# Performance work log

Hardware: AMD Instinct MI355X
Metric: run time of the kernel (lower is better)

Reference implementation:

```python
import jax, jax.numpy as jnp
import numpy as np

RTOL, ATOL = 1e-3, 1e-6
MAX_STEPS = 20          # fixed upper bound on adaptive steps (masked scan)
TA, TB, TC = 1.0, 1.0, 0.0  # trig basis params a, b, c from basis_str
B, DIN, DT, DOUT = 512, 512, 512, 512


def _rms(x):
    return jnp.sqrt(jnp.mean(x * x))


def _ode_f(t, A, C):
    # Basis.trig: stack([sin(a*A + b*t + c), cos(a*A + b*t + c)], -1) -> [B, DT, 2]
    phase = TA * A + TB * t + TC
    basis = jnp.stack([jnp.sin(phase), jnp.cos(phase)], axis=-1)
    # tensordot(A_basis, C, dims=([1,2], [1,2])): contract tensor dims + basis dim
    return jnp.einsum('bjk,ijk->bi', basis, C)


def _rk45(C, y0, t0, t1):
    """scipy-style adaptive RK45 (Dormand-Prince) from t0 to t1, fixed-length masked scan."""
    f = lambda t, y: _ode_f(t, y, C)
    f0 = f(t0, y0)
    # --- scipy _select_initial_step ---
    scale0 = ATOL + RTOL * jnp.abs(y0)
    d0 = _rms(y0 / scale0)
    d1 = _rms(f0 / scale0)
    h0 = jnp.where((d0 < 1e-5) | (d1 < 1e-5), jnp.float32(1e-6), 0.01 * d0 / d1)
    f1 = f(t0 + h0, y0 + h0 * f0)
    d2 = _rms((f1 - f0) / scale0) / h0
    dmax = jnp.maximum(d1, d2)
    h1 = jnp.where(dmax <= 1e-15, jnp.maximum(jnp.float32(1e-6), h0 * 1e-3), (0.01 / dmax) ** 0.2)
    h_init = jnp.minimum(jnp.minimum(100.0 * h0, h1), t1 - t0)

    def step(carry, _):
        t, y, fy, h, done = carry
        hs = jnp.minimum(h, t1 - t)
        k1 = fy
        k2 = f(t + hs * (1.0 / 5.0), y + hs * (k1 * (1.0 / 5.0)))
        k3 = f(t + hs * (3.0 / 10.0), y + hs * (3.0 / 40.0 * k1 + 9.0 / 40.0 * k2))
        k4 = f(t + hs * (4.0 / 5.0), y + hs * (44.0 / 45.0 * k1 - 56.0 / 15.0 * k2 + 32.0 / 9.0 * k3))
        k5 = f(t + hs * (8.0 / 9.0), y + hs * (19372.0 / 6561.0 * k1 - 25360.0 / 2187.0 * k2
                                               + 64448.0 / 6561.0 * k3 - 212.0 / 729.0 * k4))
        k6 = f(t + hs, y + hs * (9017.0 / 3168.0 * k1 - 355.0 / 33.0 * k2 + 46732.0 / 5247.0 * k3
                                 + 49.0 / 176.0 * k4 - 5103.0 / 18656.0 * k5))
        y_new = y + hs * (35.0 / 384.0 * k1 + 500.0 / 1113.0 * k3 + 125.0 / 192.0 * k4
                          - 2187.0 / 6784.0 * k5 + 11.0 / 84.0 * k6)
        k7 = f(t + hs, y_new)  # FSAL stage
        err = hs * (71.0 / 57600.0 * k1 - 71.0 / 16695.0 * k3 + 71.0 / 1920.0 * k4
                    - 17253.0 / 339200.0 * k5 + 22.0 / 525.0 * k6 - 1.0 / 40.0 * k7)
        sc = ATOL + RTOL * jnp.maximum(jnp.abs(y), jnp.abs(y_new))
        en = _rms(err / sc)
        accept = en < 1.0
        safe = jnp.maximum(en, 1e-10)
        fac = jnp.where(accept,
                        jnp.minimum(10.0, 0.9 * safe ** -0.2),
                        jnp.maximum(0.2, 0.9 * safe ** -0.2))
        t_n = jnp.where(accept, t + hs, t)
        y_n = jnp.where(accept, y_new, y)
        f_n = jnp.where(accept, k7, fy)
        h_n = hs * fac
        reached = t_n >= t1 - 1e-7
        # freeze state once integration is finished
        t_o = jnp.where(done, t, t_n)
        y_o = jnp.where(done, y, y_n)
        f_o = jnp.where(done, fy, f_n)
        h_o = jnp.where(done, h, h_n)
        return (t_o, y_o, f_o, h_o, done | reached), None

    init = (jnp.float32(t0), y0, f0, h_init.astype(jnp.float32), jnp.array(False))
    (tf, yf, _, _, _), _ = jax.lax.scan(step, init, None, length=MAX_STEPS)
    return yf


def setup_inputs() -> dict:
    key = jax.random.key(0)
    kx, kp, kc, kf = jax.random.split(key, 4)
    x = jax.random.normal(kx, (B, DIN), dtype=jnp.float32)
    P = jax.random.uniform(kp, (DIN, DT), dtype=jnp.float32, minval=0.01, maxval=1.0)
    # scale C so dA/dt stays O(1) at DT=512 (pure rescaling of the Uniform init)
    C = jax.random.uniform(kc, (DT, DT, 2), dtype=jnp.float32, minval=0.01, maxval=1.0) / (DT * 2)
    F = jax.random.uniform(kf, (DT, DOUT), dtype=jnp.float32, minval=0.01, maxval=1.0)
    return {"x": x, "P": P, "C": C, "F": F}


def reference(x, P, C, F):
    # A0 = tensordot(x, P) over input dims
    A0 = jnp.einsum('bi,ij->bj', x, P)
    Af = _rk45(C, A0, jnp.float32(0.0), jnp.float32(1.0))
    # y_hat = tensordot(A_f, F) over tensor dims
    return jnp.einsum('bj,jo->bo', Af, F)
```

## Files before the change

kernel.cpp:

```cpp
#include <hip/hip_runtime.h>
#include <cmath>

typedef float floatx4 __attribute__((ext_vector_type(4)));
typedef __bf16 bf16x8 __attribute__((ext_vector_type(8)));
typedef unsigned uintx4 __attribute__((ext_vector_type(4)));

#define NDT 512
#define NELF 262144.0f

#define AF0_OFF 16384
#define AF1_OFF (16384 + 262144)
#define BFC_OFF (16384 + 2 * 262144)
#define BFP_OFF (BFC_OFF + 262144)
#define BFF_OFF (BFP_OFF + 131072)

#define RTOLc 1e-3f
#define ATOLc 1e-6f
#define TAc 1.0f
#define TBc 1.0f
#define TCc 0.0f

union UB { uint4 u; bf16x8 v; };
union UB2 { unsigned long long q[2]; uint4 u; bf16x8 v; uintx4 x; };

__device__ __forceinline__ uint32_t f2bf(float f) {
  uint32_t u = __float_as_uint(f);
  return (u + 0x7fffu + ((u >> 16) & 1u)) >> 16;
}

#define AST(p, v) __hip_atomic_store((p), (v), __ATOMIC_RELAXED, __HIP_MEMORY_SCOPE_AGENT)
#define ALD(p) __hip_atomic_load((p), __ATOMIC_RELAXED, __HIP_MEMORY_SCOPE_AGENT)

__device__ __forceinline__ uintx4 ld128_x(const void* p) {
  uintx4 r;
  asm volatile("global_load_dwordx4 %0, %1, off sc0\n\ts_waitcnt vmcnt(0)"
               : "=v"(r) : "v"(p) : "memory");
  return r;
}

__global__ __launch_bounds__(256) void pack_all(const float* __restrict__ C,
                                                const float* __restrict__ P,
                                                const float* __restrict__ F,
                                                __bf16* __restrict__ BfC,
                                                unsigned* __restrict__ BfP,
                                                unsigned* __restrict__ BfF,
                                                unsigned* __restrict__ ctl) {
  const int bid = blockIdx.x, tid = threadIdx.x;
  if (bid == 0) {
    for (int i = tid; i < 10240; i += 256) ctl[i] = 0u;
  }
  if (bid < 512) {
    int t = bid * 256 + tid;
    int i = t >> 8;
    int pr = t & 255;
    floatx4 v = *(const floatx4*)(C + (size_t)i * 1024 + pr * 4);
    uint32_t w0 = f2bf(v[0]) | (f2bf(v[1]) << 16);
    uint32_t w1 = f2bf(v[2]) | (f2bf(v[3]) << 16);
    int c0 = i >> 4;
    int kc = pr >> 3;
    int lq = (pr >> 1) & 3;
    int ln = (i & 15) | (lq << 4);
    int jp = (pr & 1) * 4;
    uint2 val; val.x = w0; val.y = w1;
    *(uint2*)(BfC + ((size_t)(c0 * 32 + kc) * 64 + ln) * 8 + jp) = val;
  } else {
    const float* M = (bid < 640) ? P : F;
    unsigned* Bf = (bid < 640) ? BfP : BfF;
    int t = ((bid < 640) ? (bid - 512) : (bid - 640)) * 256 + tid;
    int lane = t & 63;
    int kc = (t >> 6) & 15;
    int nf = t >> 10;
    int n = nf * 16 + (lane & 15);
    int K0 = kc * 32 + ((lane >> 4) & 3) * 8;
    const float* mp = M + (size_t)K0 * NDT + n;
    uint32_t e0 = f2bf(mp[0]);
    uint32_t e1 = f2bf(mp[512]);
    uint32_t e2 = f2bf(mp[1024]);
    uint32_t e3 = f2bf(mp[1536]);
    uint32_t e4 = f2bf(mp[2048]);
    uint32_t e5 = f2bf(mp[2560]);
    uint32_t e6 = f2bf(mp[3072]);
    uint32_t e7 = f2bf(mp[3584]);
    *(uint4*)(Bf + ((size_t)(nf * 16 + kc) * 64 + lane) * 4) =
        make_uint4(e0 | (e1 << 16), e2 | (e3 << 16), e4 | (e5 << 16), e6 | (e7 << 16));
  }
}

__global__ __launch_bounds__(256, 1) void ode_mfma(const float* __restrict__ x,
                                                   float* __restrict__ out,
                                                   float* __restrict__ ws) {
  __shared__ __align__(16) float red[2][4][16][68];
  __shared__ __align__(16) unsigned short ldsX[16 * 64 * 8];
  __shared__ float bred[4];
  __shared__ float shb0s, shb1s;
  __shared__ unsigned sxc[8];

  unsigned* FLAG = (unsigned*)ws;
  float* PART1 = ws + 4096;
  unsigned long long* AfA = (unsigned long long*)(ws + AF0_OFF);
  unsigned long long* AfB = (unsigned long long*)(ws + AF1_OFF);
  unsigned long long* YF = (unsigned long long*)(ws + AF0_OFF);
  const __bf16* Bf = (const __bf16*)(ws + BFC_OFF);
  const __bf16* BfP = (const __bf16*)(ws + BFP_OFF);
  const __bf16* BfF = (const __bf16*)(ws + BFF_OFF);

  const int tid = threadIdx.x;
  const int lane = tid & 63;
  const int w = tid >> 6;
  const int cb = blockIdx.x >> 5;
  const int rg = blockIdx.x & 31;
  const int rl = tid & 15;
  const int gcq = cb * 16 + (tid >> 4);
  const int blk = rg * 8 + cb;

  bool fastp;
  {
    unsigned myxcc;
    asm volatile("s_getreg_b32 %0, hwreg(HW_REG_XCC_ID)" : "=s"(myxcc));
    myxcc &= 15u;
    if (tid == 0) AST(&FLAG[blk * 8 + 4], myxcc + 1u);
    if (tid < 8) {
      unsigned v;
      while ((v = ALD(&FLAG[(rg * 8 + tid) * 8 + 4])) == 0u) __builtin_amdgcn_s_sleep(1);
      sxc[tid] = v;
    }
    __syncthreads();
    fastp = true;
#pragma unroll
    for (int i = 0; i < 8; ++i) fastp = fastp && (sxc[i] == sxc[0]);
  }

  UB Breg[4][8];
#pragma unroll
  for (int cf = 0; cf < 4; ++cf)
#pragma unroll
    for (int i = 0; i < 8; ++i)
      Breg[cf][i].u =
          *(const uint4*)(Bf + (((size_t)(cb * 4 + cf) * 32 + 8 * w + i) * 64 + lane) * 8);

  int rg_phase = 0, par = 0, r4p = 0;

  auto rg_barrier = [&]() {
    __syncthreads();
    ++rg_phase;
    if (tid == 0) AST(&FLAG[blk * 8], (unsigned)rg_phase);
    if (tid < 8) {
      while (ALD(&FLAG[(rg * 8 + tid) * 8]) < (unsigned)rg_phase) __builtin_amdgcn_s_sleep(1);
    }
    __syncthreads();
  };

  auto reduce4 = [&](floatx4 a0, floatx4 a1, floatx4 a2, floatx4 a3) -> floatx4 {
    const int p = r4p;
    r4p ^= 1;
    const int q = lane >> 4, l4 = lane & 15;
#pragma unroll
    for (int ri = 0; ri < 4; ++ri) {
      red[p][w][4 * q + ri][l4] = a0[ri];
      red[p][w][4 * q + ri][16 + l4] = a1[ri];
      red[p][w][4 * q + ri][32 + l4] = a2[ri];
      red[p][w][4 * q + ri][48 + l4] = a3[ri];
    }
    __syncthreads();
    const int c0 = (tid >> 4) * 4;
    floatx4 o = *(const floatx4*)&red[p][0][rl][c0];
    o += *(const floatx4*)&red[p][1][rl][c0];
    o += *(const floatx4*)&red[p][2][rl][c0];
    o += *(const floatx4*)&red[p][3][rl][c0];
    return o;
  };

  const int kcw = gcq >> 2;
  const int alw = rl | ((gcq & 3) << 4);
  const size_t wslot = ((size_t)(rg * 32 + kcw) * 64 + alw) * 2;

  auto write_basis = [&](floatx4 av_, float targ) {
    uint32_t d[4];
#pragma unroll
    for (int e = 0; e < 4; ++e) {
      float s, c;
      __sincosf(TAc * av_[e] + targ, &s, &c);
      d[e] = f2bf(s) | (f2bf(c) << 16);
    }
    unsigned long long* Ap = (par ? AfB : AfA) + wslot;
    if (fastp) {
      uintx4 u = {d[0], d[1], d[2], d[3]};
      *(volatile uintx4*)Ap = u;
    } else {
      AST(Ap, (unsigned long long)d[0] | ((unsigned long long)d[1] << 32));
      AST(Ap + 1, (unsigned long long)d[2] | ((unsigned long long)d[3] << 32));
    }
  };

  auto gemm = [&]() -> floatx4 {
    const unsigned long long* Ap =
        (par ? AfB : AfA) + ((size_t)(rg * 32 + 8 * w) * 64 + lane) * 2;
    UB2 a[8];
    floatx4 acc0 = {0.f, 0.f, 0.f, 0.f}, acc1 = acc0, acc2 = acc0, acc3 = acc0;
    if (fastp) {
      const char* b0 = (const char*)Ap;
      const char* b1 = b0 + 4096;
      uintx4 t0, t1, t2, t3, t4, t5, t6, t7;
      asm volatile(
          "global_load_dwordx4 %0, %4, off sc0\n\t"
          "global_load_dwordx4 %1, %4, off offset:1024 sc0\n\t"
          "global_load_dwordx4 %2, %4, off offset:2048 sc0\n\t"
          "global_load_dwordx4 %3, %4, off offset:3072 sc0"
          : "=&v"(t0), "=&v"(t1), "=&v"(t2), "=&v"(t3)
          : "v"(b0)
          : "memory");
      asm volatile(
          "global_load_dwordx4 %0, %4, off sc0\n\t"
          "global_load_dwordx4 %1, %4, off offset:1024 sc0\n\t"
          "global_load_dwordx4 %2, %4, off offset:2048 sc0\n\t"
          "global_load_dwordx4 %3, %4, off offset:3072 sc0\n\t"
          "s_waitcnt vmcnt(4)"
          : "=&v"(t4), "=&v"(t5), "=&v"(t6), "=&v"(t7)
          : "v"(b1)
          : "memory");
      __builtin_amdgcn_sched_barrier(0);
      a[0].x = t0; a[1].x = t1; a[2].x = t2; a[3].x = t3;
#pragma unroll
      for (int i = 0; i < 4; ++i) {
        acc0 = __builtin_amdgcn_mfma_f32_16x16x32_bf16(a[i].v, Breg[0][i].v, acc0, 0, 0, 0);
        acc1 = __builtin_amdgcn_mfma_f32_16x16x32_bf16(a[i].v, Breg[1][i].v, acc1, 0, 0, 0);
        acc2 = __builtin_amdgcn_mfma_f32_16x16x32_bf16(a[i].v, Breg[2][i].v, acc2, 0, 0, 0);
        acc3 = __builtin_amdgcn_mfma_f32_16x16x32_bf16(a[i].v, Breg[3][i].v, acc3, 0, 0, 0);
      }
      asm volatile("s_waitcnt vmcnt(0)" ::: "memory");
      __builtin_amdgcn_sched_barrier(0);
      a[4].x = t4; a[5].x = t5; a[6].x = t6; a[7].x = t7;
#pragma unroll
      for (int i = 4; i < 8; ++i) {
        acc0 = __builtin_amdgcn_mfma_f32_16x16x32_bf16(a[i].v, Breg[0][i].v, acc0, 0, 0, 0);
        acc1 = __builtin_amdgcn_mfma_f32_16x16x32_bf16(a[i].v, Breg[1][i].v, acc1, 0, 0, 0);
        acc2 = __builtin_amdgcn_mfma_f32_16x16x32_bf16(a[i].v, Breg[2][i].v, acc2, 0, 0, 0);
        acc3 = __builtin_amdgcn_mfma_f32_16x16x32_bf16(a[i].v, Breg[3][i].v, acc3, 0, 0, 0);
      }
    } else {
#pragma unroll
      for (int i = 0; i < 8; ++i) {
        a[i].q[0] = ALD(Ap + (size_t)i * 128);
        a[i].q[1] = ALD(Ap + (size_t)i * 128 + 1);
      }
#pragma unroll
      for (int i = 0; i < 8; ++i) {
        acc0 = __builtin_amdgcn_mfma_f32_16x16x32_bf16(a[i].v, Breg[0][i].v, acc0, 0, 0, 0);
        acc1 = __builtin_amdgcn_mfma_f32_16x16x32_bf16(a[i].v, Breg[1][i].v, acc1, 0, 0, 0);
        acc2 = __builtin_amdgcn_mfma_f32_16x16x32_bf16(a[i].v, Breg[2][i].v, acc2, 0, 0, 0);
        acc3 = __builtin_amdgcn_mfma_f32_16x16x32_bf16(a[i].v, Breg[3][i].v, acc3, 0, 0, 0);
      }
    }
    par ^= 1;
    return reduce4(acc0, acc1, acc2, acc3);
  };

  auto block_sum = [&](float v) -> float {
#pragma unroll
    for (int o = 32; o; o >>= 1) v += __shfl_down(v, o, 64);
    __syncthreads();
    if (lane == 0) bred[w] = v;
    __syncthreads();
    return (tid == 0) ? (bred[0] + bred[1] + bred[2] + bred[3]) : 0.0f;
  };

  auto grid_reduce = [&](float va, float vb, int sa, int sb, bool two) -> float2 {
    float ba = block_sum(va);
    float bb = two ? block_sum(vb) : 0.0f;
    if (tid == 0) {
      AST((unsigned*)&PART1[sa * 256 + blk], __float_as_uint(ba) | 1u);
      if (two) AST((unsigned*)&PART1[sb * 256 + blk], __float_as_uint(bb) | 1u);
    }
    if (w == 0) {
      const unsigned* pa = (const unsigned*)&PART1[sa * 256 + lane];
      const unsigned* pb = (const unsigned*)&PART1[sb * 256 + lane];
      unsigned ua0, ua1, ua2, ua3, ub0 = 1u, ub1 = 1u, ub2 = 1u, ub3 = 1u;
      while (true) {
        ua0 = ALD(pa);
        ua1 = ALD(pa + 64);
        ua2 = ALD(pa + 128);
        ua3 = ALD(pa + 192);
        if (two) {
          ub0 = ALD(pb);
          ub1 = ALD(pb + 64);
          ub2 = ALD(pb + 128);
          ub3 = ALD(pb + 192);
        }
        if ((ua0 & ua1 & ua2 & ua3 & ub0 & ub1 & ub2 & ub3) != 0u ||
            (ua0 && ua1 && ua2 && ua3 && ub0 && ub1 && ub2 && ub3)) break;
        __builtin_amdgcn_s_sleep(1);
      }
      float x0 = __uint_as_float(ua0) + __uint_as_float(ua1) +
                 __uint_as_float(ua2) + __uint_as_float(ua3);
      float x1 = 0.0f;
      if (two)
        x1 = __uint_as_float(ub0) + __uint_as_float(ub1) +
             __uint_as_float(ub2) + __uint_as_float(ub3);
#pragma unroll
      for (int o = 32; o; o >>= 1) {
        x0 += __shfl_down(x0, o, 64);
        x1 += __shfl_down(x1, o, 64);
      }
      if (lane == 0) { shb0s = x0; shb1s = x1; }
    }
    __syncthreads();
    return make_float2(shb0s, shb1s);
  };

  floatx4 y, fy, k2, k3, k4, k5, k6, k7, yn, av;
  {
    for (int idx = tid; idx < 8192; idx += 256) {
      int r = idx >> 9, k = idx & 511;
      float v = x[(size_t)(rg * 16 + r) * NDT + k];
      int al = r | (((k >> 3) & 3) << 4);
      ldsX[((size_t)(k >> 5) * 64 + al) * 8 + (k & 7)] = (unsigned short)f2bf(v);
    }
    __syncthreads();
    floatx4 a0 = {0.f, 0.f, 0.f, 0.f}, a1 = a0, a2 = a0, a3 = a0;
#pragma unroll
    for (int i = 0; i < 4; ++i) {
      UB a, b;
      a.u = *(const uint4*)(ldsX + ((size_t)(4 * w + i) * 64 + lane) * 8);
      b.u = *(const uint4*)(BfP + (((size_t)(cb * 4 + 0) * 16 + 4 * w + i) * 64 + lane) * 8);
      a0 = __builtin_amdgcn_mfma_f32_16x16x32_bf16(a.v, b.v, a0, 0, 0, 0);
      b.u = *(const uint4*)(BfP + (((size_t)(cb * 4 + 1) * 16 + 4 * w + i) * 64 + lane) * 8);
      a1 = __builtin_amdgcn_mfma_f32_16x16x32_bf16(a.v, b.v, a1, 0, 0, 0);
      b.u = *(const uint4*)(BfP + (((size_t)(cb * 4 + 2) * 16 + 4 * w + i) * 64 + lane) * 8);
      a2 = __builtin_amdgcn_mfma_f32_16x16x32_bf16(a.v, b.v, a2, 0, 0, 0);
      b.u = *(const uint4*)(BfP + (((size_t)(cb * 4 + 3) * 16 + 4 * w + i) * 64 + lane) * 8);
      a3 = __builtin_amdgcn_mfma_f32_16x16x32_bf16(a.v, b.v, a3, 0, 0, 0);
    }
    y = reduce4(a0, a1, a2, a3);
  }

  write_basis(y, TCc + TBc * 0.0f);
  rg_barrier();
  fy = gemm();
  {
    float s0 = 0.f, s1 = 0.f;
#pragma unroll
    for (int r = 0; r < 4; ++r) {
      float sv = ATOLc + RTOLc * fabsf(y[r]);
      float a = y[r] / sv, b = fy[r] / sv;
      s0 += a * a;
      s1 += b * b;
    }
    float2 d01 = grid_reduce(s0, s1, 0, 1, true);
    const float d0 = sqrtf(d01.x / NELF);
    const float d1 = sqrtf(d01.y / NELF);
    const float h0 = (d0 < 1e-5f || d1 < 1e-5f) ? 1e-6f : 0.01f * d0 / d1;
    av = y + h0 * fy;
    write_basis(av, TCc + TBc * h0);
    rg_barrier();
    k2 = gemm();
    float s2 = 0.f;
#pragma unroll
    for (int r = 0; r < 4; ++r) {
      float sv = ATOLc + RTOLc * fabsf(y[r]);
      float dd = (k2[r] - fy[r]) / sv;
      s2 += dd * dd;
    }
    const float d2 = sqrtf(grid_reduce(s2, 0.f, 2, 0, false).x / NELF) / h0;
    const float dmax = fmaxf(d1, d2);
    const float h1i = (dmax <= 1e-15f) ? fmaxf(1e-6f, h0 * 1e-3f) : powf(0.01f / dmax, 0.2f);
    float h = fminf(fminf(100.0f * h0, h1i), 1.0f);
    float t = 0.0f;
    bool done = false;
    int it = 0;

    const float a21 = (float)(1.0 / 5.0);
    const float a31 = (float)(3.0 / 40.0), a32 = (float)(9.0 / 40.0);
    const float a41 = (float)(44.0 / 45.0), a42 = (float)(-56.0 / 15.0), a43 = (float)(32.0 / 9.0);
    const float a51 = (float)(19372.0 / 6561.0), a52 = (float)(-25360.0 / 2187.0),
                a53 = (float)(64448.0 / 6561.0), a54 = (float)(-212.0 / 729.0);
    const float a61 = (float)(9017.0 / 3168.0), a62 = (float)(-355.0 / 33.0),
                a63 = (float)(46732.0 / 5247.0), a64 = (float)(49.0 / 176.0),
                a65 = (float)(-5103.0 / 18656.0);
    const float b1 = (float)(35.0 / 384.0), b3 = (float)(500.0 / 1113.0),
                b4 = (float)(125.0 / 192.0), b5 = (float)(-2187.0 / 6784.0),
                b6 = (float)(11.0 / 84.0);
    const float e1c = (float)(71.0 / 57600.0), e3c = (float)(-71.0 / 16695.0),
                e4c = (float)(71.0 / 1920.0), e5c = (float)(-17253.0 / 339200.0),
                e6c = (float)(22.0 / 525.0), e7c = (float)(-1.0 / 40.0);
    const float c89 = (float)(8.0 / 9.0);

    while (true) {
      const float hs = fminf(h, 1.0f - t);

      av = y + (hs * a21) * fy;
      write_basis(av, TCc + TBc * (t + 0.2f * hs));
      rg_barrier();
      k2 = gemm();

      av = y + hs * (a31 * fy + a32 * k2);
      write_basis(av, TCc + TBc * (t + 0.3f * hs));
      rg_barrier();
      k3 = gemm();

      av = y + hs * (a41 * fy + a42 * k2 + a43 * k3);
      write_basis(av, TCc + TBc * (t + 0.8f * hs));
      rg_barrier();
      k4 = gemm();

      av = y + hs * (a51 * fy + a52 * k2 + a53 * k3 + a54 * k4);
      write_basis(av, TCc + TBc * (t + c89 * hs));
      rg_barrier();
      k5 = gemm();

      av = y + hs * (a61 * fy + a62 * k2 + a63 * k3 + a64 * k4 + a65 * k5);
      write_basis(av, TCc + TBc * (t + hs));
      rg_barrier();
      k6 = gemm();

      yn = y + hs * (b1 * fy + b3 * k3 + b4 * k4 + b5 * k5 + b6 * k6);
      write_basis(yn, TCc + TBc * (t + hs));
      rg_barrier();
      k7 = gemm();

      float es = 0.f;
#pragma unroll
      for (int r = 0; r < 4; ++r) {
        float errc = hs * (e1c * fy[r] + e3c * k3[r] + e4c * k4[r] + e5c * k5[r] +
                           e6c * k6[r] + e7c * k7[r]);
        float sv = ATOLc + RTOLc * fmaxf(fabsf(y[r]), fabsf(yn[r]));
        float dd = errc / sv;
        es += dd * dd;
      }
      const float en = sqrtf(grid_reduce(es, 0.f, 3 + it, 0, false).x / NELF);
      const bool accept = en < 1.0f;
      const float safe = fmaxf(en, 1e-10f);
      float fac = 0.9f * powf(safe, -0.2f);
      fac = accept ? fminf(10.0f, fac) : fmaxf(0.2f, fac);
      if (accept) {
        t = t + hs;
        y = yn;
        fy = k7;
      }
      h = hs * fac;
      done = done || (t >= 1.0f - 1e-7f);
      ++it;
      if (done || it >= 20) break;
    }
  }

  {
    uint32_t d0 = f2bf(y[0]) | (f2bf(y[1]) << 16);
    uint32_t d1 = f2bf(y[2]) | (f2bf(y[3]) << 16);
    const int kcF = gcq >> 3;
    const int alF = rl | (((gcq >> 1) & 3) << 4);
    unsigned long long* p = YF + ((size_t)(rg * 16 + kcF) * 64 + alF) * 2 + (gcq & 1);
    unsigned long long v = (unsigned long long)d0 | ((unsigned long long)d1 << 32);
    if (fastp) {
      *(volatile unsigned long long*)p = v;
    } else {
      AST(p, v);
    }
  }
  rg_barrier();
  {
    floatx4 a0 = {0.f, 0.f, 0.f, 0.f}, a1 = a0, a2 = a0, a3 = a0;
#pragma unroll
    for (int i = 0; i < 4; ++i) {
      UB2 a;
      const size_t base = ((size_t)(rg * 16 + 4 * w + i) * 64 + lane) * 2;
      if (fastp) {
        a.x = ld128_x(YF + base);
      } else {
        a.q[0] = ALD(YF + base);
        a.q[1] = ALD(YF + base + 1);
      }
      UB b;
      b.u = *(const uint4*)(BfF + (((size_t)(cb * 4 + 0) * 16 + 4 * w + i) * 64 + lane) * 8);
      a0 = __builtin_amdgcn_mfma_f32_16x16x32_bf16(a.v, b.v, a0, 0, 0, 0);
      b.u = *(const uint4*)(BfF + (((size_t)(cb * 4 + 1) * 16 + 4 * w + i) * 64 + lane) * 8);
      a1 = __builtin_amdgcn_mfma_f32_16x16x32_bf16(a.v, b.v, a1, 0, 0, 0);
      b.u = *(const uint4*)(BfF + (((size_t)(cb * 4 + 2) * 16 + 4 * w + i) * 64 + lane) * 8);
      a2 = __builtin_amdgcn_mfma_f32_16x16x32_bf16(a.v, b.v, a2, 0, 0, 0);
      b.u = *(const uint4*)(BfF + (((size_t)(cb * 4 + 3) * 16 + 4 * w + i) * 64 + lane) * 8);
      a3 = __builtin_amdgcn_mfma_f32_16x16x32_bf16(a.v, b.v, a3, 0, 0, 0);
    }
    floatx4 o = reduce4(a0, a1, a2, a3);
    *(floatx4*)(out + (size_t)(rg * 16 + rl) * NDT + cb * 64 + (tid >> 4) * 4) = o;
  }
}

extern "C" void kernel_launch(void* const* d_in, const int* in_sizes, int n_in,
                              void* d_out, int out_size, void* d_ws, size_t ws_size,
                              hipStream_t stream) {
  (void)in_sizes; (void)n_in; (void)out_size; (void)ws_size;
  const float* x = (const float*)d_in[0];
  const float* P = (const float*)d_in[1];
  const float* C = (const float*)d_in[2];
  const float* F = (const float*)d_in[3];
  float* out = (float*)d_out;
  float* ws = (float*)d_ws;

  hipLaunchKernelGGL(pack_all, dim3(768), dim3(256), 0, stream, C, P, F,
                     (__bf16*)(ws + BFC_OFF), (unsigned*)(ws + BFP_OFF),
                     (unsigned*)(ws + BFF_OFF), (unsigned*)ws);
  hipLaunchKernelGGL(ode_mfma, dim3(256), dim3(256), 0, stream, x, out, ws);
}
```

Baseline: 132.1 us.

## Fuse weight packing into the persistent ODE kernel with a grid barrier

Removes the separate pack_all launch. Each of the 256 persistent blocks now converts its share of C, P and F to bf16 MFMA layout inside the main kernel, then waits at a flag-based grid-wide barrier before the ODE solve. Control flags are zeroed with hipMemsetAsync instead of by the pack kernel. This saves one kernel launch and its gap, and lets the packing overlap the x staging into LDS. The cost is a spin barrier across all blocks, which relies on every block being resident at the same time, plus packed stores done as agent-scope atomics.

```diff
diff --git a/kernel.cpp b/kernel.cpp
--- a/kernel.cpp
+++ b/kernel.cpp
@@ -38,57 +38,12 @@
   return r;
 }
 
-__global__ __launch_bounds__(256) void pack_all(const float* __restrict__ C,
-                                                const float* __restrict__ P,
-                                                const float* __restrict__ F,
-                                                __bf16* __restrict__ BfC,
-                                                unsigned* __restrict__ BfP,
-                                                unsigned* __restrict__ BfF,
-                                                unsigned* __restrict__ ctl) {
-  const int bid = blockIdx.x, tid = threadIdx.x;
-  if (bid == 0) {
-    for (int i = tid; i < 10240; i += 256) ctl[i] = 0u;
-  }
-  if (bid < 512) {
-    int t = bid * 256 + tid;
-    int i = t >> 8;
-    int pr = t & 255;
-    floatx4 v = *(const floatx4*)(C + (size_t)i * 1024 + pr * 4);
-    uint32_t w0 = f2bf(v[0]) | (f2bf(v[1]) << 16);
-    uint32_t w1 = f2bf(v[2]) | (f2bf(v[3]) << 16);
-    int c0 = i >> 4;
-    int kc = pr >> 3;
-    int lq = (pr >> 1) & 3;
-    int ln = (i & 15) | (lq << 4);
-    int jp = (pr & 1) * 4;
-    uint2 val; val.x = w0; val.y = w1;
-    *(uint2*)(BfC + ((size_t)(c0 * 32 + kc) * 64 + ln) * 8 + jp) = val;
-  } else {
-    const float* M = (bid < 640) ? P : F;
-    unsigned* Bf = (bid < 640) ? BfP : BfF;
-    int t = ((bid < 640) ? (bid - 512) : (bid - 640)) * 256 + tid;
-    int lane = t & 63;
-    int kc = (t >> 6) & 15;
-    int nf = t >> 10;
-    int n = nf * 16 + (lane & 15);
-    int K0 = kc * 32 + ((lane >> 4) & 3) * 8;
-    const float* mp = M + (size_t)K0 * NDT + n;
-    uint32_t e0 = f2bf(mp[0]);
-    uint32_t e1 = f2bf(mp[512]);
-    uint32_t e2 = f2bf(mp[1024]);
-    uint32_t e3 = f2bf(mp[1536]);
-    uint32_t e4 = f2bf(mp[2048]);
-    uint32_t e5 = f2bf(mp[2560]);
-    uint32_t e6 = f2bf(mp[3072]);
-    uint32_t e7 = f2bf(mp[3584]);
-    *(uint4*)(Bf + ((size_t)(nf * 16 + kc) * 64 + lane) * 4) =
-        make_uint4(e0 | (e1 << 16), e2 | (e3 << 16), e4 | (e5 << 16), e6 | (e7 << 16));
-  }
-}
-
-__global__ __launch_bounds__(256, 1) void ode_mfma(const float* __restrict__ x,
-                                                   float* __restrict__ out,
-                                                   float* __restrict__ ws) {
+__global__ __launch_bounds__(256, 1) void ode_fused(const float* __restrict__ x,
+                                                    const float* __restrict__ C,
+                                                    const float* __restrict__ P,
+                                                    const float* __restrict__ F,
+                                                    float* __restrict__ out,
+                                                    float* ws) {
   __shared__ __align__(16) float red[2][4][16][68];
   __shared__ __align__(16) unsigned short ldsX[16 * 64 * 8];
   __shared__ float bred[4];
@@ -112,6 +67,76 @@
   const int rl = tid & 15;
   const int gcq = cb * 16 + (tid >> 4);
   const int blk = rg * 8 + cb;
+
+  {
+    __bf16* BfCw = (__bf16*)(ws + BFC_OFF);
+    unsigned* Bfw = (blockIdx.x < 128) ? (unsigned*)(ws + BFP_OFF)
+                                       : (unsigned*)(ws + BFF_OFF);
+#pragma unroll
+    for (int rep = 0; rep < 2; ++rep) {
+      int i = blockIdx.x * 2 + rep;
+      int pr = tid;
+      floatx4 v = *(const floatx4*)(C + (size_t)i * 1024 + pr * 4);
+      uint32_t e0 = f2bf(v[0]) | (f2bf(v[1]) << 16);
+      uint32_t e1 = f2bf(v[2]) | (f2bf(v[3]) << 16);
+      int c0 = i >> 4;
+      int kc = pr >> 3;
+      int lq = (pr >> 1) & 3;
+      int ln = (i & 15) | (lq << 4);
+      int jp = (pr & 1) * 4;
+      unsigned long long val = (unsigned long long)e0 | ((unsigned long long)e1 << 32);
+      AST((unsigned long long*)(BfCw + ((size_t)(c0 * 32 + kc) * 64 + ln) * 8 + jp), val);
+    }
+    {
+      const float* M = (blockIdx.x < 128) ? P : F;
+      int t = ((blockIdx.x < 128) ? blockIdx.x : (blockIdx.x - 128)) * 256 + tid;
+      int ln_ = t & 63;
+      int kc = (t >> 6) & 15;
+      int nf = t >> 10;
+      int n = nf * 16 + (ln_ & 15);
+      int K0 = kc * 32 + ((ln_ >> 4) & 3) * 8;
+      const float* mp = M + (size_t)K0 * NDT + n;
+      uint32_t e0 = f2bf(mp[0]);
+      uint32_t e1 = f2bf(mp[512]);
+      uint32_t e2 = f2bf(mp[1024]);
+      uint32_t e3 = f2bf(mp[1536]);
+      uint32_t e4 = f2bf(mp[2048]);
+      uint32_t e5 = f2bf(mp[2560]);
+      uint32_t e6 = f2bf(mp[3072]);
+      uint32_t e7 = f2bf(mp[3584]);
+      unsigned long long v0 =
+          (unsigned long long)(e0 | (e1 << 16)) | ((unsigned long long)(e2 | (e3 << 16)) << 32);
+      unsigned long long v1 =
+          (unsigned long long)(e4 | (e5 << 16)) | ((unsigned long long)(e6 | (e7 << 16)) << 32);
+      unsigned long long* dst =
+          (unsigned long long*)(Bfw + ((size_t)(nf * 16 + kc) * 64 + ln_) * 4);
+      AST(dst, v0);
+      AST(dst + 1, v1);
+    }
+  }
+
+  for (int idx = tid; idx < 8192; idx += 256) {
+    int r = idx >> 9, k = idx & 511;
+    float v = x[(size_t)(rg * 16 + r) * NDT + k];
+    int al = r | (((k >> 3) & 3) << 4);
+    ldsX[((size_t)(k >> 5) * 64 + al) * 8 + (k & 7)] = (unsigned short)f2bf(v);
+  }
+  __syncthreads();
+
+  {
+    if (tid == 0) AST(&FLAG[blk * 8 + 5], 1u);
+    if (w == 0) {
+      while (true) {
+        unsigned a0 = ALD(&FLAG[(lane + 0) * 8 + 5]);
+        unsigned a1 = ALD(&FLAG[(lane + 64) * 8 + 5]);
+        unsigned a2 = ALD(&FLAG[(lane + 128) * 8 + 5]);
+        unsigned a3 = ALD(&FLAG[(lane + 192) * 8 + 5]);
+        if ((a0 & a1 & a2 & a3) != 0u) break;
+        __builtin_amdgcn_s_sleep(1);
+      }
+    }
+    __syncthreads();
+  }
 
   bool fastp;
   {
@@ -309,13 +334,6 @@
 
   floatx4 y, fy, k2, k3, k4, k5, k6, k7, yn, av;
   {
-    for (int idx = tid; idx < 8192; idx += 256) {
-      int r = idx >> 9, k = idx & 511;
-      float v = x[(size_t)(rg * 16 + r) * NDT + k];
-      int al = r | (((k >> 3) & 3) << 4);
-      ldsX[((size_t)(k >> 5) * 64 + al) * 8 + (k & 7)] = (unsigned short)f2bf(v);
-    }
-    __syncthreads();
     floatx4 a0 = {0.f, 0.f, 0.f, 0.f}, a1 = a0, a2 = a0, a3 = a0;
 #pragma unroll
     for (int i = 0; i < 4; ++i) {
@@ -495,8 +513,6 @@
   float* out = (float*)d_out;
   float* ws = (float*)d_ws;
 
-  hipLaunchKernelGGL(pack_all, dim3(768), dim3(256), 0, stream, C, P, F,
-                     (__bf16*)(ws + BFC_OFF), (unsigned*)(ws + BFP_OFF),
-                     (unsigned*)(ws + BFF_OFF), (unsigned*)ws);
-  hipLaunchKernelGGL(ode_mfma, dim3(256), dim3(256), 0, stream, x, out, ws);
+  hipMemsetAsync(ws, 0, 10240 * sizeof(unsigned), stream);
+  hipLaunchKernelGGL(ode_fused, dim3(256), dim3(256), 0, stream, x, C, P, F, out, ws);
 }
```

Result: no change. 131.9 us (-0.2%).
